# Kernel tuning notes

Measured on AMD Instinct MI355X. Metric: run time of the kernel, lower is better.

Reference implementation:

```python
import jax, jax.numpy as jnp
import numpy as np

NEG_SLOPE = 0.2

def gat_layer(x, src, dst, W, a_src, a_dst, b, n_nodes):
    # x: [N, Fin]; src/dst: [E] (self-loops already appended)
    h = x @ W                                   # [N, Fout]
    s = h @ a_src                               # [N] per-node source attention term
    d = h @ a_dst                               # [N]
    e = jax.nn.leaky_relu(s[src] + d[dst], NEG_SLOPE)   # [E]
    # softmax over incoming edges of each dst node (numerically stable)
    m = jax.ops.segment_max(e, dst, num_segments=n_nodes)
    m = jnp.where(jnp.isfinite(m), m, 0.0)
    ex = jnp.exp(e - m[dst])
    z = jax.ops.segment_sum(ex, dst, num_segments=n_nodes)
    alpha = ex / z[dst]                         # [E]
    out = jax.ops.segment_sum(alpha[:, None] * h[src], dst, num_segments=n_nodes)
    return out + b

def setup_inputs() -> dict:
    key = jax.random.key(0)
    ks = jax.random.split(key, 12)
    N, E, F_IN, F_OUT = 50000, 800000, 128, 128
    H = 2 * F_OUT  # 256, conv1 output width
    x = jax.random.normal(ks[0], (N, F_IN), dtype=jnp.float32)
    edge_index = jax.random.randint(ks[1], (2, E), 0, N, dtype=jnp.int64)
    glorot = lambda k, shape: jax.random.uniform(k, shape, jnp.float32, -1.0, 1.0) * jnp.sqrt(6.0 / sum(shape))
    return {
        "x": x,
        "edge_index": edge_index,
        "W1": glorot(ks[2], (F_IN, H)),
        "a_src1": glorot(ks[3], (H,)) * 0.1,
        "a_dst1": glorot(ks[4], (H,)) * 0.1,
        "b1": jnp.zeros((H,), jnp.float32),
        "W2": glorot(ks[5], (H, F_OUT)),
        "a_src2": glorot(ks[6], (F_OUT,)) * 0.1,
        "a_dst2": glorot(ks[7], (F_OUT,)) * 0.1,
        "b2": jnp.zeros((F_OUT,), jnp.float32),
    }

def reference(x, edge_index, W1, a_src1, a_dst1, b1, W2, a_src2, a_dst2, b2):
    n_nodes = x.shape[0]
    # PyG GATConv adds self-loops by default
    loops = jnp.arange(n_nodes, dtype=edge_index.dtype)
    src = jnp.concatenate([edge_index[0], loops])
    dst = jnp.concatenate([edge_index[1], loops])
    h = gat_layer(x, src, dst, W1, a_src1, a_dst1, b1, n_nodes)
    h = jax.nn.relu(h)
    return gat_layer(h, src, dst, W2, a_src2, a_dst2, b2, n_nodes)
```

## Files before the change

### kernel.cpp

```cpp
#include <hip/hip_runtime.h>
#include <hip/hip_bf16.h>


#define NEG_SLOPE 0.2f
#define NB 104
#define EPB 8192
#define NBUCKET 1568
#define BSH 5

typedef __attribute__((ext_vector_type(8))) short bf16x8;
typedef __attribute__((ext_vector_type(4))) float f32x4;

__device__ __forceinline__ unsigned short f2bf(float v) {
    __hip_bfloat16 b = __float2bfloat16(v);
    return *reinterpret_cast<unsigned short*>(&b);
}
__device__ __forceinline__ float bf2f(unsigned short u) {
    __hip_bfloat16 b = *reinterpret_cast<__hip_bfloat16*>(&u);
    return __bfloat162float(b);
}

__global__ __launch_bounds__(256) void wprep_k(
    const float* __restrict__ W1, const float* __restrict__ W2,
    const float* __restrict__ a_src1, const float* __restrict__ a_dst1,
    unsigned short* __restrict__ w1T, unsigned short* __restrict__ w2T,
    float* __restrict__ w_s1, float* __restrict__ w_d1) {
    const int b = blockIdx.x;
    if (b < 128) {
        int i = b * 256 + threadIdx.x;
        int k = i >> 8, n = i & 255;
        w1T[n * 128 + k] = f2bf(W1[i]);
    } else if (b < 256) {
        int j = (b - 128) * 256 + threadIdx.x;
        int k = j >> 7, n = j & 127;
        w2T[n * 256 + k] = f2bf(W2[j]);
    } else {
        int w = ((b - 256) * 256 + threadIdx.x) >> 6;
        int lane = threadIdx.x & 63;
        const float* row = W1 + (size_t)w * 256;
        float ss = 0.f, dd = 0.f;
        #pragma unroll
        for (int f = lane; f < 256; f += 64) {
            float v = row[f];
            ss += v * a_src1[f];
            dd += v * a_dst1[f];
        }
        #pragma unroll
        for (int off = 32; off; off >>= 1) {
            ss += __shfl_down(ss, off);
            dd += __shfl_down(dd, off);
        }
        if (lane == 0) { w_s1[w] = ss; w_d1[w] = dd; }
    }
}

__global__ __launch_bounds__(256) void hist_xprep_k(
    const int* __restrict__ dstE, const float* __restrict__ x,
    const float* __restrict__ va, const float* __restrict__ vb,
    int* __restrict__ histG, unsigned short* __restrict__ xbf,
    float* __restrict__ s, float* __restrict__ d, int E, int N) {
    const int b = blockIdx.x;
    if (b < NB) {
        __shared__ int h[NBUCKET];
        for (int i = threadIdx.x; i < NBUCKET; i += 256) h[i] = 0;
        __syncthreads();
        const int base = b * EPB;
        const int total = E + N;
        #pragma unroll
        for (int q = 0; q < EPB / 256; ++q) {
            int i = base + q * 256 + threadIdx.x;
            if (i < total) {
                int di = (i < E) ? dstE[i] : i - E;
                atomicAdd(&h[di >> BSH], 1);
            }
        }
        __syncthreads();
        for (int i = threadIdx.x; i < NBUCKET; i += 256)
            histG[b * NBUCKET + i] = h[i];
    } else {
        int w = (((b - NB) * 256) + threadIdx.x) >> 6;
        int lane = threadIdx.x & 63;
        if (w >= N) return;
        float2 v = *(const float2*)(x + (size_t)w * 128 + lane * 2);
        ushort2 u;
        u.x = f2bf(v.x);
        u.y = f2bf(v.y);
        *(ushort2*)(xbf + (size_t)w * 128 + lane * 2) = u;
        float ss = v.x * va[lane * 2] + v.y * va[lane * 2 + 1];
        float dd = v.x * vb[lane * 2] + v.y * vb[lane * 2 + 1];
        #pragma unroll
        for (int off = 32; off; off >>= 1) {
            ss += __shfl_down(ss, off);
            dd += __shfl_down(dd, off);
        }
        if (lane == 0) { s[w] = ss; d[w] = dd; }
    }
}

__global__ __launch_bounds__(256) void colscan_k(
    int* __restrict__ histG, int* __restrict__ colSum) {
    const int bkt = blockIdx.x * 4 + (threadIdx.x >> 6);
    const int l = threadIdx.x & 63;
    int carry = 0;
    #pragma unroll
    for (int c = 0; c < 2; ++c) {
        int blk = c * 64 + l;
        int v = (blk < NB) ? histG[blk * NBUCKET + bkt] : 0;
        int incl = v;
        #pragma unroll
        for (int off = 1; off < 64; off <<= 1) {
            int t = __shfl_up(incl, off);
            if (l >= off) incl += t;
        }
        if (blk < NB) histG[blk * NBUCKET + bkt] = carry + (incl - v);
        carry += __shfl(incl, 63);
    }
    if (l == 0) colSum[bkt] = carry;
}

__global__ __launch_bounds__(256) void bucketbase_k(
    const int* __restrict__ colSum, int* __restrict__ bb, int total) {
    __shared__ int wsum[4];
    const int tid = threadIdx.x;
    const int lane = tid & 63, wv = tid >> 6;
    const int base = tid * 7;
    int loc[7];
    int s = 0;
    #pragma unroll
    for (int q = 0; q < 7; ++q) {
        int idx = base + q;
        int c = (idx < NBUCKET) ? colSum[idx] : 0;
        loc[q] = s;
        s += c;
    }
    int incl = s;
    #pragma unroll
    for (int off = 1; off < 64; off <<= 1) {
        int t = __shfl_up(incl, off);
        if (lane >= off) incl += t;
    }
    if (lane == 63) wsum[wv] = incl;
    __syncthreads();
    if (tid == 0) {
        int r = 0;
        #pragma unroll
        for (int i = 0; i < 4; ++i) { int c = wsum[i]; wsum[i] = r; r += c; }
    }
    __syncthreads();
    const int b0 = wsum[wv] + (incl - s);
    #pragma unroll
    for (int q = 0; q < 7; ++q) {
        int idx = base + q;
        if (idx < NBUCKET) bb[idx] = b0 + loc[q];
    }
    if (tid == 0) bb[NBUCKET] = total;
}

__global__ __launch_bounds__(256) void bscatter_k(
    const int* __restrict__ srcE, const int* __restrict__ dstE,
    const int* __restrict__ histG, const int* __restrict__ bb,
    unsigned* __restrict__ packed, int E, int N) {
    __shared__ int cur[NBUCKET];
    for (int i = threadIdx.x; i < NBUCKET; i += 256) cur[i] = 0;
    __syncthreads();
    const int b = blockIdx.x;
    const int base = b * EPB;
    const int total = E + N;
    #pragma unroll
    for (int q = 0; q < EPB / 256; ++q) {
        int i = base + q * 256 + threadIdx.x;
        if (i < total) {
            int di, si;
            if (i < E) { di = dstE[i]; si = srcE[i]; }
            else       { di = si = i - E; }
            int bk = di >> BSH;
            int r = atomicAdd(&cur[bk], 1);
            packed[bb[bk] + histG[b * NBUCKET + bk] + r] =
                ((unsigned)di << 16) | (unsigned)si;
        }
    }
}

__global__ __launch_bounds__(256) void bsort_k(
    const unsigned* __restrict__ packed, const int* __restrict__ bb,
    int* __restrict__ ssrc, int* __restrict__ rowptr, int N) {
    __shared__ unsigned arr[2048];
    __shared__ int cnt[32], pf[32], cur[32];
    const int b = blockIdx.x;
    const int beg = bb[b], end = bb[b + 1];
    const int L = end - beg;
    if (threadIdx.x < 32) cnt[threadIdx.x] = 0;
    __syncthreads();
    for (int t = threadIdx.x; t < L; t += 256) {
        unsigned e = packed[beg + t];
        arr[t] = e;
        atomicAdd(&cnt[(e >> 16) & 31], 1);
    }
    __syncthreads();
    if (threadIdx.x == 0) {
        int r = 0;
        #pragma unroll
        for (int j = 0; j < 32; ++j) { pf[j] = r; cur[j] = r; r += cnt[j]; }
    }
    __syncthreads();
    if (threadIdx.x < 32) {
        int dd = b * 32 + threadIdx.x;
        if (dd < N) rowptr[dd] = beg + pf[threadIdx.x];
    }
    for (int t = threadIdx.x; t < L; t += 256) {
        unsigned e = arr[t];
        int r = atomicAdd(&cur[(e >> 16) & 31], 1);
        ssrc[beg + r] = (int)(e & 0xffffu);
    }
    if (b == 0 && threadIdx.x == 0) rowptr[N] = bb[NBUCKET];
}

template <int K, int NN, int EPI>
__global__ __launch_bounds__(256) void gemm_bf16(
    const unsigned short* __restrict__ A, const unsigned short* __restrict__ BT,
    unsigned short* __restrict__ C, const float* __restrict__ bias,
    const float* __restrict__ va, const float* __restrict__ vb,
    float* __restrict__ sOut, float* __restrict__ dOut, int M) {
    constexpr int BK = 32, PAD = 8;
    __shared__ short As[128][BK + PAD];
    __shared__ short Bs[128][BK + PAD];
    const int tid = threadIdx.x;
    const int wv = tid >> 6;
    const int ln = tid & 63;
    const int row0 = blockIdx.x * 128;
    const int col0 = blockIdx.y * 128;

    f32x4 acc[2][8];
    #pragma unroll
    for (int m = 0; m < 2; ++m)
        #pragma unroll
        for (int n = 0; n < 8; ++n) acc[m][n] = {0.f, 0.f, 0.f, 0.f};

    const int l15 = ln & 15;
    const int kg = (ln >> 4) * 8;

    for (int k0 = 0; k0 < K; k0 += BK) {
        #pragma unroll
        for (int t = 0; t < 2; ++t) {
            int v = tid + t * 256;
            int r = v >> 2;
            int kc = (v & 3) * 8;
            bf16x8 val = {0, 0, 0, 0, 0, 0, 0, 0};
            int gr = row0 + r;
            if (gr < M)
                val = *(const bf16x8*)(A + (size_t)gr * K + k0 + kc);
            *(bf16x8*)(&As[r][kc]) = val;
        }
        #pragma unroll
        for (int t = 0; t < 2; ++t) {
            int v = tid + t * 256;
            int c = v >> 2;
            int kc = (v & 3) * 8;
            *(bf16x8*)(&Bs[c][kc]) =
                *(const bf16x8*)(BT + (size_t)(col0 + c) * K + k0 + kc);
        }
        __syncthreads();

        bf16x8 ah[2], bh[8];
        #pragma unroll
        for (int m = 0; m < 2; ++m)
            ah[m] = *(const bf16x8*)&As[wv * 32 + m * 16 + l15][kg];
        #pragma unroll
        for (int n = 0; n < 8; ++n)
            bh[n] = *(const bf16x8*)&Bs[n * 16 + l15][kg];
        #pragma unroll
        for (int m = 0; m < 2; ++m)
            #pragma unroll
            for (int n = 0; n < 8; ++n)
                acc[m][n] = __builtin_amdgcn_mfma_f32_16x16x32_bf16(
                    ah[m], bh[n], acc[m][n], 0, 0, 0);
        __syncthreads();
    }

    const int crow = (ln >> 4) * 4;
    #pragma unroll
    for (int m = 0; m < 2; ++m) {
        #pragma unroll
        for (int q = 0; q < 4; ++q) {
            int gr = row0 + wv * 32 + m * 16 + crow + q;
            if (gr >= M) continue;
            if constexpr (EPI == 1) {
                #pragma unroll
                for (int n = 0; n < 8; ++n) {
                    int gc = col0 + n * 16 + l15;
                    float v = acc[m][n][q] + bias[gc];
                    v = fmaxf(v, 0.f);
                    C[(size_t)gr * NN + gc] = f2bf(v);
                }
            } else {
                float sp = 0.f, dp = 0.f;
                #pragma unroll
                for (int n = 0; n < 8; ++n) {
                    int gc = n * 16 + l15;
                    float v = acc[m][n][q];
                    C[(size_t)gr * NN + gc] = f2bf(v);
                    sp += v * va[gc];
                    dp += v * vb[gc];
                }
                #pragma unroll
                for (int off = 1; off < 16; off <<= 1) {
                    sp += __shfl_xor(sp, off);
                    dp += __shfl_xor(dp, off);
                }
                if (l15 == 0) { sOut[gr] = sp; dOut[gr] = dp; }
            }
        }
    }
}

template <bool OUTBF>
__global__ __launch_bounds__(256) void node_gather_k(
    const int* __restrict__ rowptr, const int* __restrict__ ssrc,
    const float* __restrict__ s, const float* __restrict__ d,
    const unsigned short* __restrict__ hsrc, const float* __restrict__ bias,
    unsigned short* __restrict__ obf, float* __restrict__ outf, int N) {
    constexpr int F = 128, G = 8;
    const int node = blockIdx.x * 4 + (threadIdx.x >> 6);
    const int lane = threadIdx.x & 63;
    if (node >= N) return;
    const int beg = rowptr[node];
    const int end = rowptr[node + 1];
    const float dn = d[node];
    const int grp = lane >> 3;
    const int lr = lane & 7;

    float acc[16] = {};
    float zsum = 0.f;
    int j = beg + grp;
    for (; j + G < end; j += 2 * G) {
        int sj0 = ssrc[j];
        int sj1 = ssrc[j + G];
        float e0 = s[sj0] + dn;
        float e1 = s[sj1] + dn;
        const unsigned short* r0 = hsrc + (size_t)sj0 * F + lr * 16;
        const unsigned short* r1 = hsrc + (size_t)sj1 * F + lr * 16;
        bf16x8 v0a = *(const bf16x8*)r0;
        bf16x8 v0b = *(const bf16x8*)(r0 + 8);
        bf16x8 v1a = *(const bf16x8*)r1;
        bf16x8 v1b = *(const bf16x8*)(r1 + 8);
        e0 = (e0 > 0.f) ? e0 : NEG_SLOPE * e0;
        e1 = (e1 > 0.f) ? e1 : NEG_SLOPE * e1;
        float x0 = __expf(e0);
        float x1 = __expf(e1);
        zsum += x0 + x1;
        #pragma unroll
        for (int q = 0; q < 8; ++q) {
            acc[q]     += x0 * bf2f(((unsigned short*)&v0a)[q]);
            acc[q + 8] += x0 * bf2f(((unsigned short*)&v0b)[q]);
            acc[q]     += x1 * bf2f(((unsigned short*)&v1a)[q]);
            acc[q + 8] += x1 * bf2f(((unsigned short*)&v1b)[q]);
        }
    }
    if (j < end) {
        int sj = ssrc[j];
        float e = s[sj] + dn;
        e = (e > 0.f) ? e : NEG_SLOPE * e;
        float exj = __expf(e);
        zsum += exj;
        const unsigned short* r0 = hsrc + (size_t)sj * F + lr * 16;
        bf16x8 va_ = *(const bf16x8*)r0;
        bf16x8 vb_ = *(const bf16x8*)(r0 + 8);
        #pragma unroll
        for (int q = 0; q < 8; ++q) {
            acc[q]     += exj * bf2f(((unsigned short*)&va_)[q]);
            acc[q + 8] += exj * bf2f(((unsigned short*)&vb_)[q]);
        }
    }
    #pragma unroll
    for (int off = 8; off < 64; off <<= 1) {
        zsum += __shfl_xor(zsum, off);
        #pragma unroll
        for (int q = 0; q < 16; ++q) acc[q] += __shfl_xor(acc[q], off);
    }
    const float inv = 1.f / zsum;

    if (lane < 8) {
        if constexpr (OUTBF) {
            bf16x8 w0, w1;
            #pragma unroll
            for (int q = 0; q < 8; ++q) {
                ((unsigned short*)&w0)[q] = f2bf(acc[q] * inv);
                ((unsigned short*)&w1)[q] = f2bf(acc[q + 8] * inv);
            }
            *(bf16x8*)(obf + (size_t)node * F + lr * 16) = w0;
            *(bf16x8*)(obf + (size_t)node * F + lr * 16 + 8) = w1;
        } else {
            float o[16];
            #pragma unroll
            for (int q = 0; q < 16; ++q)
                o[q] = acc[q] * inv + bias[lr * 16 + q];
            float* op = outf + (size_t)node * F + lr * 16;
            *(float4*)op = {o[0], o[1], o[2], o[3]};
            *(float4*)(op + 4) = {o[4], o[5], o[6], o[7]};
            *(float4*)(op + 8) = {o[8], o[9], o[10], o[11]};
            *(float4*)(op + 12) = {o[12], o[13], o[14], o[15]};
        }
    }
}

extern "C" void kernel_launch(void* const* d_in, const int* in_sizes, int n_in,
                              void* d_out, int out_size, void* d_ws, size_t ws_size,
                              hipStream_t stream) {
    const float* x      = (const float*)d_in[0];
    const int*   eidx   = (const int*)d_in[1];
    const float* W1     = (const float*)d_in[2];
    const float* a_src1 = (const float*)d_in[3];
    const float* a_dst1 = (const float*)d_in[4];
    const float* b1     = (const float*)d_in[5];
    const float* W2     = (const float*)d_in[6];
    const float* a_src2 = (const float*)d_in[7];
    const float* a_dst2 = (const float*)d_in[8];
    const float* b2     = (const float*)d_in[9];

    const int N = in_sizes[0] / 128;
    const int E = in_sizes[1] / 2;
    const int F_IN = 128, H = 256, F_OUT = 128;
    const int EA = E + N;

    const int* srcE = eidx;
    const int* dstE = eidx + E;

    unsigned short* xbf    = (unsigned short*)d_ws;
    unsigned short* aggx   = xbf + (size_t)N * F_IN;
    unsigned short* g1     = aggx + (size_t)N * F_IN;
    unsigned short* h2bf   = g1 + (size_t)N * H;
    float*          sbuf   = (float*)(h2bf + (size_t)N * F_OUT);
    float*          dbuf   = sbuf + N;
    float*          w_s1   = dbuf + N;
    float*          w_d1   = w_s1 + F_IN;
    unsigned short* w1T    = (unsigned short*)(w_d1 + F_IN);
    unsigned short* w2T    = w1T + 32768;
    int*            rowptr = (int*)(w2T + 32768);
    int*            histG  = rowptr + (N + 1);
    int*            colSum = histG + NB * NBUCKET;
    int*            bb     = colSum + NBUCKET;
    int*            ssrc   = bb + NBUCKET + 1;
    unsigned*       packed = (unsigned*)(ssrc + EA);

    float* out = (float*)d_out;
    const int xblocks = (N * 64 + 255) / 256;

    wprep_k<<<288, 256, 0, stream>>>(W1, W2, a_src1, a_dst1, w1T, w2T, w_s1, w_d1);
    hist_xprep_k<<<NB + xblocks, 256, 0, stream>>>(
        dstE, x, w_s1, w_d1, histG, xbf, sbuf, dbuf, E, N);
    colscan_k<<<NBUCKET / 4, 256, 0, stream>>>(histG, colSum);
    bucketbase_k<<<1, 256, 0, stream>>>(colSum, bb, EA);
    bscatter_k<<<NB, 256, 0, stream>>>(srcE, dstE, histG, bb, packed, E, N);
    bsort_k<<<NBUCKET, 256, 0, stream>>>(packed, bb, ssrc, rowptr, N);

    {
        int nb = (N + 3) / 4;
        node_gather_k<true><<<nb, 256, 0, stream>>>(
            rowptr, ssrc, sbuf, dbuf, xbf, nullptr, aggx, nullptr, N);
    }
    {
        dim3 gg((N + 127) / 128, H / 128);
        gemm_bf16<128, 256, 1><<<gg, 256, 0, stream>>>(
            aggx, w1T, g1, b1, nullptr, nullptr, nullptr, nullptr, N);
    }
    {
        dim3 gg((N + 127) / 128, 1);
        gemm_bf16<256, 128, 2><<<gg, 256, 0, stream>>>(
            g1, w2T, h2bf, nullptr, a_src2, a_dst2, sbuf, dbuf, N);
    }
    {
        int nb = (N + 3) / 4;
        node_gather_k<false><<<nb, 256, 0, stream>>>(
            rowptr, ssrc, sbuf, dbuf, h2bf, b2, nullptr, out, N);
    }
}
```

Measured before the change: 155.5 us.

## Merge preprocessing kernels and fold bucket-base scan into scatter and sort

Weight prep is folded into the histogram kernel and the x bf16 conversion plus s/d projection into the column-scan kernel. The single-block bucket-base scan is dropped: each scatter block recomputes the bucket prefix sum in shared memory, and each sort block sums colSum up to its index to find its start. This cuts two kernel launches and their serial dependency gaps. In exchange every scatter block repeats the 1568-entry scan and each sort block does a reduction over up to 1568 entries.

```diff
diff --git a/kernel.cpp b/kernel.cpp
--- a/kernel.cpp
+++ b/kernel.cpp
@@ -20,45 +20,12 @@
     return __bfloat162float(b);
 }
 
-__global__ __launch_bounds__(256) void wprep_k(
-    const float* __restrict__ W1, const float* __restrict__ W2,
-    const float* __restrict__ a_src1, const float* __restrict__ a_dst1,
+__global__ __launch_bounds__(256) void hist_wprep_k(
+    const int* __restrict__ dstE, const float* __restrict__ W1,
+    const float* __restrict__ W2, const float* __restrict__ a_src1,
+    const float* __restrict__ a_dst1, int* __restrict__ histG,
     unsigned short* __restrict__ w1T, unsigned short* __restrict__ w2T,
-    float* __restrict__ w_s1, float* __restrict__ w_d1) {
-    const int b = blockIdx.x;
-    if (b < 128) {
-        int i = b * 256 + threadIdx.x;
-        int k = i >> 8, n = i & 255;
-        w1T[n * 128 + k] = f2bf(W1[i]);
-    } else if (b < 256) {
-        int j = (b - 128) * 256 + threadIdx.x;
-        int k = j >> 7, n = j & 127;
-        w2T[n * 256 + k] = f2bf(W2[j]);
-    } else {
-        int w = ((b - 256) * 256 + threadIdx.x) >> 6;
-        int lane = threadIdx.x & 63;
-        const float* row = W1 + (size_t)w * 256;
-        float ss = 0.f, dd = 0.f;
-        #pragma unroll
-        for (int f = lane; f < 256; f += 64) {
-            float v = row[f];
-            ss += v * a_src1[f];
-            dd += v * a_dst1[f];
-        }
-        #pragma unroll
-        for (int off = 32; off; off >>= 1) {
-            ss += __shfl_down(ss, off);
-            dd += __shfl_down(dd, off);
-        }
-        if (lane == 0) { w_s1[w] = ss; w_d1[w] = dd; }
-    }
-}
-
-__global__ __launch_bounds__(256) void hist_xprep_k(
-    const int* __restrict__ dstE, const float* __restrict__ x,
-    const float* __restrict__ va, const float* __restrict__ vb,
-    int* __restrict__ histG, unsigned short* __restrict__ xbf,
-    float* __restrict__ s, float* __restrict__ d, int E, int N) {
+    float* __restrict__ w_s1, float* __restrict__ w_d1, int E, int N) {
     const int b = blockIdx.x;
     if (b < NB) {
         __shared__ int h[NBUCKET];
@@ -77,8 +44,61 @@
         __syncthreads();
         for (int i = threadIdx.x; i < NBUCKET; i += 256)
             histG[b * NBUCKET + i] = h[i];
+    } else if (b < NB + 128) {
+        int i = (b - NB) * 256 + threadIdx.x;
+        int k = i >> 8, n = i & 255;
+        w1T[n * 128 + k] = f2bf(W1[i]);
+    } else if (b < NB + 256) {
+        int j = (b - NB - 128) * 256 + threadIdx.x;
+        int k = j >> 7, n = j & 127;
+        w2T[n * 256 + k] = f2bf(W2[j]);
     } else {
-        int w = (((b - NB) * 256) + threadIdx.x) >> 6;
+        int w = ((b - NB - 256) * 256 + threadIdx.x) >> 6;
+        int lane = threadIdx.x & 63;
+        const float* row = W1 + (size_t)w * 256;
+        float ss = 0.f, dd = 0.f;
+        #pragma unroll
+        for (int f = lane; f < 256; f += 64) {
+            float v = row[f];
+            ss += v * a_src1[f];
+            dd += v * a_dst1[f];
+        }
+        #pragma unroll
+        for (int off = 32; off; off >>= 1) {
+            ss += __shfl_down(ss, off);
+            dd += __shfl_down(dd, off);
+        }
+        if (lane == 0) { w_s1[w] = ss; w_d1[w] = dd; }
+    }
+}
+
+__global__ __launch_bounds__(256) void colscan_xprep_k(
+    int* __restrict__ histG, int* __restrict__ colSum,
+    const float* __restrict__ x, const float* __restrict__ va,
+    const float* __restrict__ vb, unsigned short* __restrict__ xbf,
+    float* __restrict__ s, float* __restrict__ d, int N) {
+    const int b = blockIdx.x;
+    constexpr int CSB = NBUCKET / 4;
+    if (b < CSB) {
+        const int bkt = b * 4 + (threadIdx.x >> 6);
+        const int l = threadIdx.x & 63;
+        int carry = 0;
+        #pragma unroll
+        for (int c = 0; c < 2; ++c) {
+            int blk = c * 64 + l;
+            int v = (blk < NB) ? histG[blk * NBUCKET + bkt] : 0;
+            int incl = v;
+            #pragma unroll
+            for (int off = 1; off < 64; off <<= 1) {
+                int t = __shfl_up(incl, off);
+                if (l >= off) incl += t;
+            }
+            if (blk < NB) histG[blk * NBUCKET + bkt] = carry + (incl - v);
+            carry += __shfl(incl, 63);
+        }
+        if (l == 0) colSum[bkt] = carry;
+    } else {
+        int w = (((b - CSB) * 256) + threadIdx.x) >> 6;
         int lane = threadIdx.x & 63;
         if (w >= N) return;
         float2 v = *(const float2*)(x + (size_t)w * 128 + lane * 2);
@@ -97,122 +117,111 @@
     }
 }
 
-__global__ __launch_bounds__(256) void colscan_k(
-    int* __restrict__ histG, int* __restrict__ colSum) {
-    const int bkt = blockIdx.x * 4 + (threadIdx.x >> 6);
-    const int l = threadIdx.x & 63;
-    int carry = 0;
-    #pragma unroll
-    for (int c = 0; c < 2; ++c) {
-        int blk = c * 64 + l;
-        int v = (blk < NB) ? histG[blk * NBUCKET + bkt] : 0;
-        int incl = v;
+__global__ __launch_bounds__(256) void bscatter_k(
+    const int* __restrict__ srcE, const int* __restrict__ dstE,
+    const int* __restrict__ histG, const int* __restrict__ colSum,
+    unsigned* __restrict__ packed, int E, int N) {
+    __shared__ int bb_s[NBUCKET];
+    __shared__ int cur[NBUCKET];
+    __shared__ int wsum[4];
+    const int tid = threadIdx.x;
+    {
+        const int lane = tid & 63, wv = tid >> 6;
+        const int base = tid * 7;
+        int loc[7];
+        int ssum = 0;
+        #pragma unroll
+        for (int q = 0; q < 7; ++q) {
+            int idx = base + q;
+            int c = (idx < NBUCKET) ? colSum[idx] : 0;
+            loc[q] = ssum;
+            ssum += c;
+        }
+        int incl = ssum;
         #pragma unroll
         for (int off = 1; off < 64; off <<= 1) {
             int t = __shfl_up(incl, off);
-            if (l >= off) incl += t;
-        }
-        if (blk < NB) histG[blk * NBUCKET + bkt] = carry + (incl - v);
-        carry += __shfl(incl, 63);
-    }
-    if (l == 0) colSum[bkt] = carry;
-}
-
-__global__ __launch_bounds__(256) void bucketbase_k(
-    const int* __restrict__ colSum, int* __restrict__ bb, int total) {
-    __shared__ int wsum[4];
-    const int tid = threadIdx.x;
-    const int lane = tid & 63, wv = tid >> 6;
-    const int base = tid * 7;
-    int loc[7];
-    int s = 0;
-    #pragma unroll
-    for (int q = 0; q < 7; ++q) {
-        int idx = base + q;
-        int c = (idx < NBUCKET) ? colSum[idx] : 0;
-        loc[q] = s;
-        s += c;
-    }
-    int incl = s;
-    #pragma unroll
-    for (int off = 1; off < 64; off <<= 1) {
-        int t = __shfl_up(incl, off);
-        if (lane >= off) incl += t;
-    }
-    if (lane == 63) wsum[wv] = incl;
-    __syncthreads();
-    if (tid == 0) {
-        int r = 0;
-        #pragma unroll
-        for (int i = 0; i < 4; ++i) { int c = wsum[i]; wsum[i] = r; r += c; }
-    }
-    __syncthreads();
-    const int b0 = wsum[wv] + (incl - s);
-    #pragma unroll
-    for (int q = 0; q < 7; ++q) {
-        int idx = base + q;
-        if (idx < NBUCKET) bb[idx] = b0 + loc[q];
-    }
-    if (tid == 0) bb[NBUCKET] = total;
-}
-
-__global__ __launch_bounds__(256) void bscatter_k(
-    const int* __restrict__ srcE, const int* __restrict__ dstE,
-    const int* __restrict__ histG, const int* __restrict__ bb,
-    unsigned* __restrict__ packed, int E, int N) {
-    __shared__ int cur[NBUCKET];
-    for (int i = threadIdx.x; i < NBUCKET; i += 256) cur[i] = 0;
+            if (lane >= off) incl += t;
+        }
+        if (lane == 63) wsum[wv] = incl;
+        __syncthreads();
+        if (tid == 0) {
+            int r = 0;
+            #pragma unroll
+            for (int i = 0; i < 4; ++i) { int c = wsum[i]; wsum[i] = r; r += c; }
+        }
+        __syncthreads();
+        const int b0 = wsum[wv] + (incl - ssum);
+        #pragma unroll
+        for (int q = 0; q < 7; ++q) {
+            int idx = base + q;
+            if (idx < NBUCKET) bb_s[idx] = b0 + loc[q];
+        }
+    }
+    for (int i = tid; i < NBUCKET; i += 256) cur[i] = 0;
     __syncthreads();
     const int b = blockIdx.x;
     const int base = b * EPB;
     const int total = E + N;
     #pragma unroll
     for (int q = 0; q < EPB / 256; ++q) {
-        int i = base + q * 256 + threadIdx.x;
+        int i = base + q * 256 + tid;
         if (i < total) {
             int di, si;
             if (i < E) { di = dstE[i]; si = srcE[i]; }
             else       { di = si = i - E; }
             int bk = di >> BSH;
             int r = atomicAdd(&cur[bk], 1);
-            packed[bb[bk] + histG[b * NBUCKET + bk] + r] =
+            packed[bb_s[bk] + histG[b * NBUCKET + bk] + r] =
                 ((unsigned)di << 16) | (unsigned)si;
         }
     }
 }
 
 __global__ __launch_bounds__(256) void bsort_k(
-    const unsigned* __restrict__ packed, const int* __restrict__ bb,
-    int* __restrict__ ssrc, int* __restrict__ rowptr, int N) {
+    const unsigned* __restrict__ packed, const int* __restrict__ colSum,
+    int* __restrict__ ssrc, int* __restrict__ rowptr, int EA, int N) {
     __shared__ unsigned arr[2048];
     __shared__ int cnt[32], pf[32], cur[32];
+    __shared__ int red[4];
+    __shared__ int beg_s;
     const int b = blockIdx.x;
-    const int beg = bb[b], end = bb[b + 1];
-    const int L = end - beg;
-    if (threadIdx.x < 32) cnt[threadIdx.x] = 0;
+    const int tid = threadIdx.x;
+    {
+        int part = 0;
+        for (int i = tid; i < b; i += 256) part += colSum[i];
+        #pragma unroll
+        for (int off = 32; off; off >>= 1) part += __shfl_down(part, off);
+        if ((tid & 63) == 0) red[tid >> 6] = part;
+        __syncthreads();
+        if (tid == 0) beg_s = red[0] + red[1] + red[2] + red[3];
+    }
+    if (tid < 32) cnt[tid] = 0;
     __syncthreads();
-    for (int t = threadIdx.x; t < L; t += 256) {
+    const int beg = beg_s;
+    const int L = colSum[b];
+    for (int t = tid; t < L; t += 256) {
         unsigned e = packed[beg + t];
         arr[t] = e;
         atomicAdd(&cnt[(e >> 16) & 31], 1);
     }
     __syncthreads();
-    if (threadIdx.x == 0) {
+    if (tid == 0) {
         int r = 0;
         #pragma unroll
         for (int j = 0; j < 32; ++j) { pf[j] = r; cur[j] = r; r += cnt[j]; }
     }
     __syncthreads();
-    if (threadIdx.x < 32) {
-        int dd = b * 32 + threadIdx.x;
-        if (dd < N) rowptr[dd] = beg + pf[threadIdx.x];
-    }
-    for (int t = threadIdx.x; t < L; t += 256) {
+    if (tid < 32) {
+        int dd = b * 32 + tid;
+        if (dd < N) rowptr[dd] = beg + pf[tid];
+    }
+    for (int t = tid; t < L; t += 256) {
         unsigned e = arr[t];
         int r = atomicAdd(&cur[(e >> 16) & 31], 1);
         ssrc[beg + r] = (int)(e & 0xffffu);
     }
-    if (b == 0 && threadIdx.x == 0) rowptr[N] = bb[NBUCKET];
+    if (b == 0 && tid == 0) rowptr[N] = EA;
 }
 
 template <int K, int NN, int EPI>
@@ -438,20 +447,18 @@
     int*            rowptr = (int*)(w2T + 32768);
     int*            histG  = rowptr + (N + 1);
     int*            colSum = histG + NB * NBUCKET;
-    int*            bb     = colSum + NBUCKET;
-    int*            ssrc   = bb + NBUCKET + 1;
+    int*            ssrc   = colSum + NBUCKET;
     unsigned*       packed = (unsigned*)(ssrc + EA);
 
     float* out = (float*)d_out;
     const int xblocks = (N * 64 + 255) / 256;
 
-    wprep_k<<<288, 256, 0, stream>>>(W1, W2, a_src1, a_dst1, w1T, w2T, w_s1, w_d1);
-    hist_xprep_k<<<NB + xblocks, 256, 0, stream>>>(
-        dstE, x, w_s1, w_d1, histG, xbf, sbuf, dbuf, E, N);
-    colscan_k<<<NBUCKET / 4, 256, 0, stream>>>(histG, colSum);
-    bucketbase_k<<<1, 256, 0, stream>>>(colSum, bb, EA);
-    bscatter_k<<<NB, 256, 0, stream>>>(srcE, dstE, histG, bb, packed, E, N);
-    bsort_k<<<NBUCKET, 256, 0, stream>>>(packed, bb, ssrc, rowptr, N);
+    hist_wprep_k<<<NB + 288, 256, 0, stream>>>(
+        dstE, W1, W2, a_src1, a_dst1, histG, w1T, w2T, w_s1, w_d1, E, N);
+    colscan_xprep_k<<<NBUCKET / 4 + xblocks, 256, 0, stream>>>(
+        histG, colSum, x, w_s1, w_d1, xbf, sbuf, dbuf, N);
+    bscatter_k<<<NB, 256, 0, stream>>>(srcE, dstE, histG, colSum, packed, E, N);
+    bsort_k<<<NBUCKET, 256, 0, stream>>>(packed, colSum, ssrc, rowptr, EA, N);
 
     {
         int nb = (N + 3) / 4;
```

After: 153.9 us. Within noise of the previous version (-1.0%).
